# Kernel optimization log

Hardware: AMD Instinct MI355X
Metric: run time of the kernel (lower is better)

## Reference

```python
import jax, jax.numpy as jnp
import numpy as np
from jax import lax

ALPHA = 0.5
KERNEL = 25
NUM_P = 16
SEQ_LEN = 1440
PRED_LEN = 720
DWT_LEN = SEQ_LEN // 2 + 2            # 722 (pytorch_wavelets zero-mode, sym3 filt len 6)
FREQ = int(np.ceil(DWT_LEN / 2 * ALPHA) * 2)  # 362

_DEC_LO = np.array([0.035226291882100656, -0.08544127388224149, -0.13501102001039084,
                    0.4598775021193313, 0.8068915093133388, 0.3326705529509569], np.float32)
_DEC_HI = np.array([-0.3326705529509569, 0.8068915093133388, -0.4598775021193313,
                    -0.13501102001039084, 0.08544127388224149, 0.035226291882100656], np.float32)
DEC_LO, DEC_HI = jnp.asarray(_DEC_LO), jnp.asarray(_DEC_HI)
REC_LO, REC_HI = DEC_LO[::-1], DEC_HI[::-1]


def dwt1(x):
    # pytorch_wavelets DWT1DForward(J=1, mode='zero'): zero-pad then stride-2 true conv with dec filters
    B, C, L = x.shape
    out = (L + 5) // 2
    p = 2 * (out - 1) - L + 6
    xp = jnp.pad(x.reshape(B * C, 1, L), ((0, 0), (0, 0), (p // 2, p - p // 2)))
    ker = jnp.stack([DEC_LO[::-1], DEC_HI[::-1]])[:, None, :]   # (2,1,6); xcorr w/ reversed == conv
    y = lax.conv_general_dilated(xp, ker, (2,), 'VALID', dimension_numbers=('NCH', 'OIH', 'NCH'))
    return y[:, 0].reshape(B, C, out), y[:, 1].reshape(B, C, out)


def iwt1(lo, hi):
    # DWT1DInverse mode='zero': conv_transpose stride 2, padding L-2  ->  dilate + conv, pad 1
    B, C, n = lo.shape
    z = jnp.concatenate([lo.reshape(B * C, 1, n), hi.reshape(B * C, 1, n)], axis=1)
    ker = jnp.stack([REC_LO[::-1], REC_HI[::-1]])[None, :, :]   # (O=1, I=2, 6)
    y = lax.conv_general_dilated(z, ker, (1,), [(1, 1)], lhs_dilation=(2,),
                                 dimension_numbers=('NCH', 'OIH', 'NCH'))
    return y[:, 0].reshape(B, C, 2 * n - 4)


def mov_avg(x, k=KERNEL):
    pooled = lax.reduce_window(x, 0.0, lax.add, (1, 1, k), (1, 1, 1), 'VALID') / k
    return jnp.pad(pooled, ((0, 0), (0, 0), (k // 2, k // 2 - (k + 1) % 2)), mode='edge')


def mov_norm(x):
    mean = lax.stop_gradient(mov_avg(x))
    xc = lax.stop_gradient(x - mean)
    std = lax.stop_gradient(mov_avg(jnp.abs(xc))) + 1e-5
    return xc / std, mean, std


def inst_norm(x):
    mean = lax.stop_gradient(jnp.mean(x, -1, keepdims=True))
    xc = x - mean
    var = jnp.mean((xc - jnp.mean(xc, -1, keepdims=True)) ** 2, -1, keepdims=True)
    return xc / jnp.sqrt(var + 1e-5)


def mean_std_mlp(mean, std, mp, sp, mw1, mw2, sw1, sw2, mpred, spred):
    m_all = jnp.mean(mean, -1, keepdims=True)
    s_all = jnp.mean(std, -1, keepdims=True)
    mr = (mean - m_all) @ mp.T
    sr = (std - s_all) @ sp.T
    mr = jax.nn.relu(mr @ mw1.T) @ mw2.T
    sr = jax.nn.relu(sr @ sw1.T) @ sw2.T
    mean_o = mr @ mpred.T + m_all
    std_o = jax.nn.relu(sr @ spred.T + s_all) + 1e-5
    return mean_o, std_o


def forward(x, latent_w, latent_b, acp, dcp):
    xt = jnp.swapaxes(x, -1, 1)                    # (B, C, L)
    ac0, dc0 = dwt1(xt)                            # (B, C, DWT_LEN)
    ac_n = inst_norm(ac0)
    ac, m_ac, s_ac = mov_norm(ac0)
    dc, m_dc, s_dc = mov_norm(dc0)
    m_ac, s_ac = mean_std_mlp(m_ac, s_ac, *acp)    # MLPs[-1]
    m_dc, s_dc = mean_std_mlp(m_dc, s_dc, *dcp)    # MLPs[0]
    dcF = jnp.fft.fft(dc)
    acF = jnp.fft.fft(ac_n)
    idx = jnp.argsort(-jnp.abs(acF), axis=-1)[..., :FREQ]
    amp = ALPHA * jnp.take_along_axis(acF, idx, -1) + (1.0 - ALPHA) * jnp.take_along_axis(dcF, idx, -1)
    B, C, _ = dcF.shape
    bi = jnp.arange(B)[:, None, None]
    ci = jnp.arange(C)[None, :, None]
    dcF = dcF.at[bi, ci, idx].set(amp)
    dc = jnp.real(jnp.fft.ifft(dcF))
    xr = iwt1(ac, dc)                              # (B, C, SEQ_LEN)
    mean = iwt1(m_ac, m_dc)                        # (B, C, PRED_LEN)
    std = iwt1(s_ac, s_dc)
    xr = xr.reshape(B, C, NUM_P, SEQ_LEN // NUM_P)
    emb = xr @ latent_w.T + latent_b               # (B, C, NUM_P, d_model)
    return emb, mean, std


def setup_inputs() -> dict:
    key = jax.random.key(0)
    B, C = 64, 128
    d_model, d_ff = 512, 1024
    s = 0.02
    names_shapes = [
        ('x', (B, SEQ_LEN, C), 1.0),
        ('latent_w', (d_model, SEQ_LEN // NUM_P), s),
    ]
    for pre in ('ac', 'dc'):
        names_shapes += [
            (pre + '_mean_proj', (d_model, DWT_LEN), s),
            (pre + '_std_proj', (d_model, DWT_LEN), s),
            (pre + '_mean_ffn_w1', (d_ff, d_model), s),
            (pre + '_mean_ffn_w2', (d_model, d_ff), s),
            (pre + '_std_ffn_w1', (d_ff, d_model), s),
            (pre + '_std_ffn_w2', (d_model, d_ff), s),
            (pre + '_mean_pred', (PRED_LEN // 2 + 2, d_model), s),
            (pre + '_std_pred', (PRED_LEN // 2 + 2, d_model), s),
        ]
    keys = jax.random.split(key, len(names_shapes))
    inp = {n: jax.random.normal(k, shp, dtype=jnp.float32) * sc
           for (n, shp, sc), k in zip(names_shapes, keys)}
    inp['latent_b'] = jnp.zeros((d_model,), jnp.float32)
    return inp


def reference(x, latent_w, latent_b,
              ac_mean_proj, ac_std_proj, ac_mean_ffn_w1, ac_mean_ffn_w2,
              ac_std_ffn_w1, ac_std_ffn_w2, ac_mean_pred, ac_std_pred,
              dc_mean_proj, dc_std_proj, dc_mean_ffn_w1, dc_mean_ffn_w2,
              dc_std_ffn_w1, dc_std_ffn_w2, dc_mean_pred, dc_std_pred):
    acp = (ac_mean_proj, ac_std_proj, ac_mean_ffn_w1, ac_mean_ffn_w2,
           ac_std_ffn_w1, ac_std_ffn_w2, ac_mean_pred, ac_std_pred)
    dcp = (dc_mean_proj, dc_std_proj, dc_mean_ffn_w1, dc_mean_ffn_w2,
           dc_std_ffn_w1, dc_std_ffn_w2, dc_mean_pred, dc_std_pred)
    return forward(x, latent_w, latent_b, acp, dcp)
```

## Files before the change

kernel.cpp:

```cpp
#include <hip/hip_runtime.h>
#include <cmath>

#define RTOT 8192
#define NDWT 722
#define KP1  736
#define LSEQ 1440
#define NHEAD 362
#define NFREQ 362

typedef __bf16 bf16x8 __attribute__((ext_vector_type(8)));
typedef float f32x4 __attribute__((ext_vector_type(4)));
typedef float f32x2 __attribute__((ext_vector_type(2)));

__device__ __forceinline__ unsigned short f2bf(float f) {
    unsigned u = __float_as_uint(f);
    u += 0x7fffu + ((u >> 16) & 1u);
    return (unsigned short)(u >> 16);
}
__device__ __forceinline__ float bf2f(unsigned short u) {
    return __uint_as_float(((unsigned)u) << 16);
}

__device__ __forceinline__ void cmac(f32x2& s, f32x2 a, f32x2 w) {
    asm("v_pk_fma_f32 %0, %1, %2, %0 op_sel:[0,0,0] op_sel_hi:[0,1,1]\n\t"
        "v_pk_fma_f32 %0, %1, %2, %0 op_sel:[1,1,0] op_sel_hi:[1,0,1] neg_lo:[0,1,0]"
        : "+v"(s) : "v"(a), "v"(w));
}
__device__ __forceinline__ f32x2 cmul(f32x2 a, f32x2 b) {
    f32x2 r;
    asm("v_pk_mul_f32 %0, %1, %2 op_sel:[0,0] op_sel_hi:[0,1]\n\t"
        "v_pk_fma_f32 %0, %1, %2, %0 op_sel:[1,1,0] op_sel_hi:[1,0,1] neg_lo:[0,1,0]"
        : "=&v"(r) : "v"(a), "v"(b));
    return r;
}

__constant__ float c_lo[6] = {0.035226291882100656f, -0.08544127388224149f, -0.13501102001039084f,
                              0.4598775021193313f, 0.8068915093133388f, 0.3326705529509569f};
__constant__ float c_hi[6] = {-0.3326705529509569f, 0.8068915093133388f, -0.4598775021193313f,
                              -0.13501102001039084f, 0.08544127388224149f, 0.035226291882100656f};

__global__ void wtab_kernel(float2* __restrict__ Wtab) {
    int m = blockIdx.x * blockDim.x + threadIdx.x;
    if (m < NDWT) {
        double ang = -2.0 * 3.141592653589793238462643383279502884 * (double)m / (double)NDWT;
        Wtab[m] = make_float2((float)cos(ang), (float)sin(ang));
    }
}

struct CvtDesc { const float* src; unsigned short* dst; int N, K, Np, Kp; };
struct CvtArgs { CvtDesc d[17]; };
__global__ __launch_bounds__(256) void cvt_all_kernel(CvtArgs a) {
    CvtDesc d = a.d[blockIdx.y];
    int idx = blockIdx.x * 256 + threadIdx.x;
    int tot = d.Np * d.Kp;
    if (idx >= tot) return;
    int r = idx / d.Kp, c = idx - r * d.Kp;
    float v = (r < d.N && c < d.K) ? d.src[(size_t)r * d.K + c] : 0.f;
    d.dst[idx] = f2bf(v);
}

__global__ __launch_bounds__(256) void dwt_kernel(const float* __restrict__ x,
                                                  float* __restrict__ ac0,
                                                  float* __restrict__ dc0) {
    __shared__ float xs[68][129];
    const int b = blockIdx.x;
    const int t0 = blockIdx.y * 32;
    const int tid = threadIdx.x;
    const int lbase = 2 * t0 - 4;
    for (int i = tid; i < 68 * 32; i += 256) {
        int ri = i >> 5;
        int c4 = (i & 31) * 4;
        int l = lbase + ri;
        float4 v = make_float4(0.f, 0.f, 0.f, 0.f);
        if (l >= 0 && l < LSEQ)
            v = *reinterpret_cast<const float4*>(&x[((size_t)b * LSEQ + l) * 128 + c4]);
        xs[ri][c4] = v.x; xs[ri][c4 + 1] = v.y; xs[ri][c4 + 2] = v.z; xs[ri][c4 + 3] = v.w;
    }
    __syncthreads();
    const int tt = tid & 31;
    const int t = t0 + tt;
    const int cw = tid >> 5;
    if (t < NDWT) {
        #pragma unroll 4
        for (int co = 0; co < 16; co++) {
            int c = co * 8 + cw;
            float slo = 0.f, shi = 0.f;
            #pragma unroll
            for (int j = 0; j < 6; j++) {
                float v = xs[2 * tt + 5 - j][c];
                slo += v * c_lo[j];
                shi += v * c_hi[j];
            }
            size_t o = ((size_t)b * 128 + c) * NDWT + t;
            ac0[o] = slo;
            dc0[o] = shi;
        }
    }
}

__device__ __forceinline__ float blockSum256(float v, float* red) {
    #pragma unroll
    for (int o = 32; o > 0; o >>= 1) v += __shfl_down(v, o, 64);
    int lane = threadIdx.x & 63, wid = threadIdx.x >> 6;
    __syncthreads();
    if (lane == 0) red[wid] = v;
    __syncthreads();
    return red[0] + red[1] + red[2] + red[3];
}

template <bool ABS>
__device__ __forceinline__ void pool25(const float* rowv, float* pool, int tid) {
    int i0 = tid * 3;
    if (i0 < 698) {
        float s25 = 0.f;
        #pragma unroll
        for (int j = 0; j < 25; j++) { float v = rowv[i0 + j]; s25 += ABS ? fabsf(v) : v; }
        pool[i0] = s25 * (1.f / 25.f);
        #pragma unroll
        for (int qq = 1; qq < 3; qq++) {
            int i = i0 + qq;
            if (i < 698) {
                float vin = rowv[i + 24], vout = rowv[i - 1];
                s25 += (ABS ? fabsf(vin) : vin) - (ABS ? fabsf(vout) : vout);
                pool[i] = s25 * (1.f / 25.f);
            }
        }
    }
}

__global__ __launch_bounds__(256) void rowstats_kernel(
    const float* __restrict__ ac0in, const float* __restrict__ dc0in,
    float* __restrict__ acn,
    float* __restrict__ acp,
    float* __restrict__ dcp,
    unsigned short* __restrict__ cent,
    float* __restrict__ stat ) {
    __shared__ float row[NDWT];
    __shared__ float xc[NDWT];
    __shared__ float pool[698];
    __shared__ float red[4];
    const int r = blockIdx.x, tid = threadIdx.x;
    const size_t base = (size_t)r * NDWT;
    const size_t baseP = (size_t)r * KP1;
    const size_t CS = (size_t)RTOT * KP1;

    if (blockIdx.y == 0) {
        for (int i = tid; i < NDWT; i += 256) row[i] = ac0in[base + i];
        __syncthreads();
        float s = 0.f;
        for (int i = tid; i < NDWT; i += 256) s += row[i];
        float mean = blockSum256(s, red) * (1.f / 722.f);
        s = 0.f;
        for (int i = tid; i < NDWT; i += 256) s += row[i] - mean;
        float m2 = blockSum256(s, red) * (1.f / 722.f);
        s = 0.f;
        for (int i = tid; i < NDWT; i += 256) { float d = row[i] - mean - m2; s += d * d; }
        float var = blockSum256(s, red) * (1.f / 722.f);
        float inv = 1.f / sqrtf(var + 1e-5f);
        for (int i = tid; i < NDWT; i += 256) acn[base + i] = (row[i] - mean) * inv;

        pool25<false>(row, pool, tid);
        __syncthreads();
        float msum = 0.f;
        for (int l = tid; l < NDWT; l += 256) {
            int pi = l - 12; pi = pi < 0 ? 0 : (pi > 697 ? 697 : pi);
            float m = pool[pi];
            msum += m;
            xc[l] = row[l] - m;
        }
        float m_all = blockSum256(msum, red) * (1.f / 722.f);
        __syncthreads();
        pool25<true>(xc, pool, tid);
        __syncthreads();
        float ssum = 0.f;
        for (int l = tid; l < NDWT; l += 256) {
            int pi = l - 12; pi = pi < 0 ? 0 : (pi > 697 ? 697 : pi);
            float sd = pool[pi] + 1e-5f;
            ssum += sd;
            acp[base + l] = xc[l] / sd;
        }
        float s_all = blockSum256(ssum, red) * (1.f / 722.f);
        if (tid == 0) { stat[r] = m_all; stat[RTOT + r] = s_all; }
        for (int l = tid; l < KP1; l += 256) {
            if (l < NDWT) {
                float m = row[l] - xc[l];
                int pi = l - 12; pi = pi < 0 ? 0 : (pi > 697 ? 697 : pi);
                float sd = pool[pi] + 1e-5f;
                cent[baseP + l]      = f2bf(m - m_all);
                cent[CS + baseP + l] = f2bf(sd - s_all);
            } else { cent[baseP + l] = 0; cent[CS + baseP + l] = 0; }
        }
    } else {
        for (int i = tid; i < NDWT; i += 256) row[i] = dc0in[base + i];
        __syncthreads();
        pool25<false>(row, pool, tid);
        __syncthreads();
        float msum2 = 0.f;
        for (int l = tid; l < NDWT; l += 256) {
            int pi = l - 12; pi = pi < 0 ? 0 : (pi > 697 ? 697 : pi);
            float m = pool[pi];
            msum2 += m;
            xc[l] = row[l] - m;
        }
        float m_all2 = blockSum256(msum2, red) * (1.f / 722.f);
        __syncthreads();
        pool25<true>(xc, pool, tid);
        __syncthreads();
        float ssum2 = 0.f;
        for (int l = tid; l < NDWT; l += 256) {
            int pi = l - 12; pi = pi < 0 ? 0 : (pi > 697 ? 697 : pi);
            float sd = pool[pi] + 1e-5f;
            ssum2 += sd;
            dcp[base + l] = xc[l] / sd;
        }
        float s_all2 = blockSum256(ssum2, red) * (1.f / 722.f);
        if (tid == 0) { stat[2 * RTOT + r] = m_all2; stat[3 * RTOT + r] = s_all2; }
        for (int l = tid; l < KP1; l += 256) {
            if (l < NDWT) {
                float m = row[l] - xc[l];
                int pi = l - 12; pi = pi < 0 ? 0 : (pi > 697 ? 697 : pi);
                float sd = pool[pi] + 1e-5f;
                cent[2 * CS + baseP + l] = f2bf(m - m_all2);
                cent[3 * CS + baseP + l] = f2bf(sd - s_all2);
            } else { cent[2 * CS + baseP + l] = 0; cent[3 * CS + baseP + l] = 0; }
        }
    }
}

__device__ void fft722_dev(f32x2* X, f32x2* T, const f32x2* Wt, const f32x2* W19) {
    const int tid = threadIdx.x;
    if (tid < 190) {
        const int c = tid / 38;
        const int g = tid - c * 38;
        const int p = (g >= 19) ? 1 : 0;
        const int rr = g - 19 * p;
        const int t0 = c * 4;
        const int nt = (c == 4) ? 3 : 4;
        const f32x2* xp = X + 2 * rr + p;
        f32x2 st[4], w[4], s[4];
        #pragma unroll
        for (int i = 0; i < 4; i++) {
            int ti = t0 + i; if (ti > 18) ti = 0;
            st[i] = W19[ti];
            w[i] = f32x2{1.f, 0.f};
            s[i] = f32x2{0.f, 0.f};
        }
        for (int j = 0; j < 19; j++) {
            f32x2 a = xp[38 * j];
            #pragma unroll
            for (int i = 0; i < 4; i++) { cmac(s[i], a, w[i]); w[i] = cmul(w[i], st[i]); }
        }
        f32x2* Tp = T + p * 361 + rr * 19 + t0;
        #pragma unroll
        for (int i = 0; i < 4; i++) if (i < nt) Tp[i] = s[i];
    }
    __syncthreads();
    if (tid < 190) {
        const int c = tid / 38;
        const int g = tid - c * 38;
        const int p = (g >= 19) ? 1 : 0;
        const int t = g - 19 * p;
        const int j0 = c * 4;
        const int nj = (c == 4) ? 3 : 4;
        const f32x2* Tp = T + p * 361 + t;
        int kk[4];
        f32x2 st[4], w[4], s[4];
        #pragma unroll
        for (int i = 0; i < 4; i++) {
            int jj = j0 + i;
            kk[i] = (jj > 18) ? 0 : (t + 19 * jj);
            st[i] = Wt[2 * kk[i]];
            w[i] = f32x2{1.f, 0.f};
            s[i] = f32x2{0.f, 0.f};
        }
        for (int rr = 0; rr < 19; rr++) {
            f32x2 a = Tp[19 * rr];
            #pragma unroll
            for (int i = 0; i < 4; i++) { cmac(s[i], a, w[i]); w[i] = cmul(w[i], st[i]); }
        }
        f32x2* Xp = X + p * 361;
        #pragma unroll
        for (int i = 0; i < 4; i++) if (i < nj) Xp[kk[i]] = s[i];
    }
    __syncthreads();
    for (int k = tid; k < 361; k += 256) {
        f32x2 e = X[k], o = X[361 + k], w = Wt[k];
        f32x2 tt = {0.f, 0.f};
        cmac(tt, o, w);
        X[k] = e + tt;
        X[361 + k] = e - tt;
    }
    __syncthreads();
}

__global__ __launch_bounds__(256) void fft_mix_kernel(const float* __restrict__ acn,
                                                      float* __restrict__ dcp,
                                                      const f32x2* __restrict__ Wtab) {
    __shared__ f32x2 Wt[NDWT];
    __shared__ f32x2 W19s[19];
    __shared__ f32x2 B1[NDWT];
    __shared__ f32x2 B2[NDWT];
    __shared__ float smag[NDWT];
    __shared__ unsigned hist[256];
    __shared__ unsigned suf[256];
    __shared__ unsigned sh_digit, sh_rem;
    const int r = blockIdx.x, tid = threadIdx.x;
    const size_t base = (size_t)r * NDWT;

    for (int i = tid; i < NDWT; i += 256) Wt[i] = Wtab[i];
    if (tid < 19) W19s[tid] = Wtab[38 * tid];
    for (int i = tid; i < NDWT; i += 256) B1[i] = f32x2{acn[base + i], dcp[base + i]};
    __syncthreads();
    fft722_dev(B1, B2, Wt, W19s);
    for (int k = tid; k < 362; k += 256) {
        int m = (NDWT - k) % NDWT;
        f32x2 zk = B1[k], zm = B1[m];
        f32x2 ak = {0.5f * (zk.x + zm.x), 0.5f * (zk.y - zm.y)};
        f32x2 dk = {0.5f * (zk.y + zm.y), 0.5f * (zm.x - zk.x)};
        B1[k] = ak; B2[k] = dk;
        smag[k] = ak.x * ak.x + ak.y * ak.y;
        if (m != k) {
            f32x2 am = {0.5f * (zm.x + zk.x), 0.5f * (zm.y - zk.y)};
            f32x2 dm = {0.5f * (zm.y + zk.y), 0.5f * (zk.x - zm.x)};
            B1[m] = am; B2[m] = dm;
            smag[m] = am.x * am.x + am.y * am.y;
        }
    }
    __syncthreads();

    unsigned prefix = 0, rem = NFREQ;
    for (int shift = 24; shift >= 0; shift -= 8) {
        hist[tid] = 0;
        __syncthreads();
        unsigned hm = (shift == 24) ? 0u : (0xFFFFFFFFu << (shift + 8));
        for (int i = tid; i < NDWT; i += 256) {
            unsigned b = __float_as_uint(smag[i]);
            if ((b & hm) == prefix) atomicAdd(&hist[(b >> shift) & 255], 1u);
        }
        __syncthreads();
        suf[tid] = hist[tid];
        __syncthreads();
        for (int off = 1; off < 256; off <<= 1) {
            unsigned v = (tid + off < 256) ? suf[tid + off] : 0;
            __syncthreads();
            suf[tid] += v;
            __syncthreads();
        }
        unsigned Shere = suf[tid];
        unsigned Snext = (tid < 255) ? suf[tid + 1] : 0;
        if (Shere >= rem && Snext < rem) { sh_digit = (unsigned)tid; sh_rem = rem - Snext; }
        __syncthreads();
        prefix |= (sh_digit << shift);
        rem = sh_rem;
        __syncthreads();
    }
    int c0 = tid * 3, cnt = 0;
    #pragma unroll
    for (int j = 0; j < 3; j++) {
        int i = c0 + j;
        if (i < NDWT && __float_as_uint(smag[i]) == prefix) cnt++;
    }
    suf[tid] = (unsigned)cnt;
    __syncthreads();
    for (int off = 1; off < 256; off <<= 1) {
        unsigned v = (tid >= off) ? suf[tid - off] : 0;
        __syncthreads();
        suf[tid] += v;
        __syncthreads();
    }
    int myexc = (int)suf[tid] - cnt, o = 0;
    #pragma unroll
    for (int j = 0; j < 3; j++) {
        int i = c0 + j;
        if (i < NDWT) {
            unsigned b = __float_as_uint(smag[i]);
            int f = (b > prefix) ? 1 : 0;
            if (b == prefix) { if ((unsigned)(myexc + o) < rem) f = 1; o++; }
            smag[i] = f ? 1.f : 0.f;
        }
    }
    __syncthreads();

    for (int i = tid; i < NDWT; i += 256) {
        f32x2 d = B2[i];
        if (smag[i] != 0.f) { f32x2 a = B1[i]; d.x = 0.5f * (a.x + d.x); d.y = 0.5f * (a.y + d.y); }
        B1[i] = f32x2{d.x, -d.y};
    }
    __syncthreads();
    fft722_dev(B1, B2, Wt, W19s);
    for (int i = tid; i < NDWT; i += 256) dcp[base + i] = B1[i].x * (1.f / 722.f);
}

__global__ __launch_bounds__(256) void iwt_heads_kernel(const unsigned short* __restrict__ heads,
                                                        float* __restrict__ out_mean,
                                                        float* __restrict__ out_std) {
    const int z = blockIdx.z;
    const int r = blockIdx.x;
    const int t = blockIdx.y * 256 + threadIdx.x;
    if (t >= 720) return;
    const size_t HR = (size_t)RTOT * NHEAD;
    const unsigned short* lp = heads + (size_t)z * HR + (size_t)r * NHEAD;
    const unsigned short* hp = heads + (size_t)(2 + z) * HR + (size_t)r * NHEAD;
    float* out = (z ? out_std : out_mean) + (size_t)r * 720;
    float s = 0.f;
    if (t & 1) {
        int j0 = (t - 1) >> 1;
        #pragma unroll
        for (int i = 0; i < 3; i++) s += bf2f(lp[j0 + i]) * c_lo[2 * i] + bf2f(hp[j0 + i]) * c_hi[2 * i];
    } else {
        int j0 = t >> 1;
        #pragma unroll
        for (int i = 0; i < 3; i++) s += bf2f(lp[j0 + i]) * c_lo[2 * i + 1] + bf2f(hp[j0 + i]) * c_hi[2 * i + 1];
    }
    out[t] = s;
}

__global__ __launch_bounds__(256) void iwt_xr_kernel(const float* __restrict__ lo,
                                                     const float* __restrict__ hi,
                                                     unsigned short* __restrict__ xrbf) {
    const int r = blockIdx.x;
    const int t = blockIdx.y * 256 + threadIdx.x;
    if (blockIdx.y == 0 && threadIdx.x < 96) {
        int sub = threadIdx.x / 6, c = 90 + threadIdx.x % 6;
        xrbf[((size_t)r * 16 + sub) * 96 + c] = 0;
    }
    if (t >= LSEQ) return;
    const float* lp = lo + (size_t)r * NDWT;
    const float* hp = hi + (size_t)r * NDWT;
    float s = 0.f;
    if (t & 1) {
        int j0 = (t - 1) >> 1;
        #pragma unroll
        for (int i = 0; i < 3; i++) s += lp[j0 + i] * c_lo[2 * i] + hp[j0 + i] * c_hi[2 * i];
    } else {
        int j0 = t >> 1;
        #pragma unroll
        for (int i = 0; i < 3; i++) s += lp[j0 + i] * c_lo[2 * i + 1] + hp[j0 + i] * c_hi[2 * i + 1];
    }
    xrbf[((size_t)r * 16 + t / 90) * 96 + (t % 90)] = f2bf(s);
}

struct ZPtrs { const unsigned short* p[4]; };
template <int EPI>
__global__ __launch_bounds__(256) void mfma_gemm_z(
    const unsigned short* __restrict__ A, int lda, size_t zsA,
    ZPtrs Wz, int ldw,
    void* __restrict__ Cout, int ldc, size_t zsC, int Nc,
    const float* __restrict__ biasBase, const float* __restrict__ cbias,
    int Ksteps) {
    __shared__ unsigned short As[2][128 * 32];
    __shared__ unsigned short Bs[2][128 * 32];
    const int z = blockIdx.z;
    const unsigned short* Az = A + (size_t)z * zsA;
    const unsigned short* W = Wz.p[z];
    const int tid = threadIdx.x;
    const int lane = tid & 63, wid = tid >> 6;
    const int bm = blockIdx.x * 128, bn = blockIdx.y * 128;
    const int wr = (wid >> 1) * 64, wc = (wid & 1) * 64;
    f32x4 acc[4][4] = {};
    const int srow = (lane >> 2);
    const int scol = (lane & 3) * 8;
    const int ch0 = wid * 2, ch1 = wid * 2 + 1;
    const unsigned short* ga0 = Az + (size_t)(bm + ch0 * 16 + srow) * lda + scol;
    const unsigned short* ga1 = Az + (size_t)(bm + ch1 * 16 + srow) * lda + scol;
    const unsigned short* gb0 = W + (size_t)(bn + ch0 * 16 + srow) * ldw + scol;
    const unsigned short* gb1 = W + (size_t)(bn + ch1 * 16 + srow) * ldw + scol;

#define STAGE_GL(buf, ks) do { const int k0_ = (ks) * 32;                                      \
    __builtin_amdgcn_global_load_lds((const __attribute__((address_space(1))) unsigned int*)(ga0 + k0_), \
        (__attribute__((address_space(3))) unsigned int*)(&As[buf][ch0 * 512]), 16, 0, 0);     \
    __builtin_amdgcn_global_load_lds((const __attribute__((address_space(1))) unsigned int*)(gb0 + k0_), \
        (__attribute__((address_space(3))) unsigned int*)(&Bs[buf][ch0 * 512]), 16, 0, 0);     \
    __builtin_amdgcn_global_load_lds((const __attribute__((address_space(1))) unsigned int*)(ga1 + k0_), \
        (__attribute__((address_space(3))) unsigned int*)(&As[buf][ch1 * 512]), 16, 0, 0);     \
    __builtin_amdgcn_global_load_lds((const __attribute__((address_space(1))) unsigned int*)(gb1 + k0_), \
        (__attribute__((address_space(3))) unsigned int*)(&Bs[buf][ch1 * 512]), 16, 0, 0);     \
    } while (0)

    STAGE_GL(0, 0);
    int cur = 0;
    const int kof = (lane >> 4) * 8;
    for (int ks = 0; ks < Ksteps; ks++) {
        if (ks + 1 < Ksteps) {
            STAGE_GL(cur ^ 1, ks + 1);
            asm volatile("s_waitcnt vmcnt(4)" ::: "memory");
        } else {
            asm volatile("s_waitcnt vmcnt(0)" ::: "memory");
        }
        __builtin_amdgcn_s_barrier();
        __builtin_amdgcn_sched_barrier(0);
        bf16x8 af[4], bfr[4];
        #pragma unroll
        for (int m = 0; m < 4; m++)
            af[m] = *reinterpret_cast<const bf16x8*>(&As[cur][(wr + m * 16 + (lane & 15)) * 32 + kof]);
        #pragma unroll
        for (int n = 0; n < 4; n++)
            bfr[n] = *reinterpret_cast<const bf16x8*>(&Bs[cur][(wc + n * 16 + (lane & 15)) * 32 + kof]);
        #pragma unroll
        for (int m = 0; m < 4; m++)
            #pragma unroll
            for (int n = 0; n < 4; n++)
                acc[m][n] = __builtin_amdgcn_mfma_f32_16x16x32_bf16(af[m], bfr[n], acc[m][n], 0, 0, 0);
        __builtin_amdgcn_s_barrier();
        __builtin_amdgcn_sched_barrier(0);
        cur ^= 1;
    }
#undef STAGE_GL

    unsigned short* Cb = (unsigned short*)Cout + (size_t)z * zsC;
    float* Cf = (float*)Cout + (size_t)z * zsC;
    const int crow0 = bm + wr + (lane >> 4) * 4;
    const int ccol0 = bn + wc + (lane & 15);
    #pragma unroll
    for (int m = 0; m < 4; m++) {
        #pragma unroll
        for (int n = 0; n < 4; n++) {
            const int col = ccol0 + n * 16;
            if (col < Nc) {
                #pragma unroll
                for (int q = 0; q < 4; q++) {
                    const int row = crow0 + m * 16 + q;
                    float v = acc[m][n][q];
                    if (EPI == 0) {
                        Cb[(size_t)row * ldc + col] = f2bf(v);
                    } else if (EPI == 1) {
                        Cb[(size_t)row * ldc + col] = f2bf(fmaxf(v, 0.f));
                    } else if (EPI == 4) {
                        Cf[(size_t)row * ldc + col] = v + cbias[col];
                    } else {
                        float ob = biasBase[(size_t)z * RTOT + row];
                        if (z & 1) v = fmaxf(v + ob, 0.f) + 1e-5f;
                        else       v += ob;
                        Cb[(size_t)row * ldc + col] = f2bf(v);
                    }
                }
            }
        }
    }
}

extern "C" void kernel_launch(void* const* d_in, const int* in_sizes, int n_in,
                              void* d_out, int out_size, void* d_ws, size_t ws_size,
                              hipStream_t stream) {
    const float* x = (const float*)d_in[0];
    const float* latent_w = (const float*)d_in[1];
    int p0;
    const float* latent_b;
    if (n_in > 2 && in_sizes[2] == 512) { latent_b = (const float*)d_in[2]; p0 = 3; }
    else                                { latent_b = (const float*)d_in[18]; p0 = 2; }

    char* wp = (char*)d_ws;
    auto alloc = [&](size_t bytes) { char* p = wp; wp += (bytes + 255) & ~(size_t)255; return p; };
    const size_t RN = (size_t)RTOT * NDWT;
    float* acn  = (float*)alloc(RN * 4);
    float* dcb  = (float*)alloc(RN * 4);
    float* acp  = (float*)alloc(RN * 4);
    float* stat = (float*)alloc(4 * RTOT * 4);
    float2* Wtab = (float2*)alloc(NDWT * 8);
    unsigned short* cent  = (unsigned short*)alloc((size_t)4 * RTOT * KP1 * 2);
    unsigned short* mlpB4 = (unsigned short*)alloc((size_t)4 * RTOT * 512 * 2);
    unsigned short* mlpA4 = (unsigned short*)alloc((size_t)4 * RTOT * 1024 * 2);
    unsigned short* mlpC4 = (unsigned short*)alloc((size_t)4 * RTOT * 512 * 2);
    unsigned short* heads = mlpB4;
    unsigned short* xrbf = mlpC4;
    unsigned short *projW[4], *w1W[4], *w2W[4], *predW[4];
    for (int z = 0; z < 4; z++) {
        projW[z] = (unsigned short*)alloc((size_t)512 * KP1 * 2);
        w1W[z]   = (unsigned short*)alloc((size_t)1024 * 512 * 2);
        w2W[z]   = (unsigned short*)alloc((size_t)512 * 1024 * 2);
        predW[z] = (unsigned short*)alloc((size_t)384 * 512 * 2);
    }
    unsigned short* latwb = (unsigned short*)alloc((size_t)512 * 96 * 2);
    (void)ws_size;

    CvtArgs ca;
    int si = 0;
    for (int z = 0; z < 4; z++) {
        int branch = z >> 1, isStd = z & 1, wb = p0 + branch * 8;
        ca.d[si++] = {(const float*)d_in[wb + isStd],         projW[z], 512, NDWT, 512, KP1};
        ca.d[si++] = {(const float*)d_in[wb + 2 + 2 * isStd], w1W[z], 1024, 512, 1024, 512};
        ca.d[si++] = {(const float*)d_in[wb + 3 + 2 * isStd], w2W[z], 512, 1024, 512, 1024};
        ca.d[si++] = {(const float*)d_in[wb + 6 + isStd],     predW[z], NHEAD, 512, 384, 512};
    }
    ca.d[16] = {latent_w, latwb, 512, 90, 512, 96};
    cvt_all_kernel<<<dim3(2048, 17), dim3(256), 0, stream>>>(ca);

    wtab_kernel<<<dim3(3), dim3(256), 0, stream>>>(Wtab);
    dwt_kernel<<<dim3(64, 23), dim3(256), 0, stream>>>(x, acn, dcb);
    rowstats_kernel<<<dim3(RTOT, 2), dim3(256), 0, stream>>>(acn, dcb, acn, acp, dcb, cent, stat);
    fft_mix_kernel<<<dim3(RTOT), dim3(256), 0, stream>>>(acn, dcb, (const f32x2*)Wtab);

    ZPtrs Zp = {{projW[0], projW[1], projW[2], projW[3]}};
    ZPtrs Z1 = {{w1W[0], w1W[1], w1W[2], w1W[3]}};
    ZPtrs Z2 = {{w2W[0], w2W[1], w2W[2], w2W[3]}};
    ZPtrs Zh = {{predW[0], predW[1], predW[2], predW[3]}};
    mfma_gemm_z<0><<<dim3(64, 4, 4), dim3(256), 0, stream>>>(
        cent, KP1, (size_t)RTOT * KP1, Zp, KP1, mlpB4, 512, (size_t)RTOT * 512, 512, nullptr, nullptr, KP1 / 32);
    mfma_gemm_z<1><<<dim3(64, 8, 4), dim3(256), 0, stream>>>(
        mlpB4, 512, (size_t)RTOT * 512, Z1, 512, mlpA4, 1024, (size_t)RTOT * 1024, 1024, nullptr, nullptr, 16);
    mfma_gemm_z<0><<<dim3(64, 4, 4), dim3(256), 0, stream>>>(
        mlpA4, 1024, (size_t)RTOT * 1024, Z2, 1024, mlpC4, 512, (size_t)RTOT * 512, 512, nullptr, nullptr, 32);
    mfma_gemm_z<5><<<dim3(64, 3, 4), dim3(256), 0, stream>>>(
        mlpC4, 512, (size_t)RTOT * 512, Zh, 512, heads, NHEAD, (size_t)RTOT * NHEAD, NHEAD, stat, nullptr, 16);

    float* out = (float*)d_out;
    float* out_mean = out + (size_t)67108864;
    float* out_std  = out_mean + (size_t)5898240;
    iwt_heads_kernel<<<dim3(RTOT, 3, 2), dim3(256), 0, stream>>>(heads, out_mean, out_std);
    iwt_xr_kernel<<<dim3(RTOT, 6), dim3(256), 0, stream>>>(acp, dcb, xrbf);

    ZPtrs Zl = {{latwb, latwb, latwb, latwb}};
    mfma_gemm_z<4><<<dim3(1024, 4, 1), dim3(256), 0, stream>>>(
        xrbf, 96, 0, Zl, 96, out, 512, 0, 512, nullptr, latent_b, 3);
}
```

Before: 539.3 us.

## Exploit conjugate symmetry in FFT722 DFT stages and merge small kernels

Both 19-point DFT stages now pair inputs m and 19-m into sum and difference terms, so each complex MAC covers two inputs and the loop count halves. The first stage applies its twiddle on output instead of carrying it through the second stage's recurrence. The twiddle-table kernel is folded into the weight-conversion launch, and the two inverse-wavelet kernels are merged into one launch. This removes FFT arithmetic and two launches, at the cost of more complex index math and slightly different rounding.

```diff
diff --git a/kernel.cpp b/kernel.cpp
--- a/kernel.cpp
+++ b/kernel.cpp
@@ -26,6 +26,11 @@
         "v_pk_fma_f32 %0, %1, %2, %0 op_sel:[1,1,0] op_sel_hi:[1,0,1] neg_lo:[0,1,0]"
         : "+v"(s) : "v"(a), "v"(w));
 }
+__device__ __forceinline__ void cmac2(f32x2& s, f32x2 u, f32x2 v, f32x2 w) {
+    asm("v_pk_fma_f32 %0, %1, %3, %0 op_sel:[0,0,0] op_sel_hi:[1,0,1]\n\t"
+        "v_pk_fma_f32 %0, %2, %3, %0 op_sel:[1,1,0] op_sel_hi:[0,1,1] neg_lo:[0,1,0]"
+        : "+v"(s) : "v"(u), "v"(v), "v"(w));
+}
 __device__ __forceinline__ f32x2 cmul(f32x2 a, f32x2 b) {
     f32x2 r;
     asm("v_pk_mul_f32 %0, %1, %2 op_sel:[0,0] op_sel_hi:[0,1]\n\t"
@@ -39,17 +44,17 @@
 __constant__ float c_hi[6] = {-0.3326705529509569f, 0.8068915093133388f, -0.4598775021193313f,
                               -0.13501102001039084f, 0.08544127388224149f, 0.035226291882100656f};
 
-__global__ void wtab_kernel(float2* __restrict__ Wtab) {
-    int m = blockIdx.x * blockDim.x + threadIdx.x;
-    if (m < NDWT) {
-        double ang = -2.0 * 3.141592653589793238462643383279502884 * (double)m / (double)NDWT;
-        Wtab[m] = make_float2((float)cos(ang), (float)sin(ang));
-    }
-}
-
 struct CvtDesc { const float* src; unsigned short* dst; int N, K, Np, Kp; };
-struct CvtArgs { CvtDesc d[17]; };
+struct CvtArgs { CvtDesc d[17]; float2* wtab; };
 __global__ __launch_bounds__(256) void cvt_all_kernel(CvtArgs a) {
+    if (blockIdx.y == 17) {
+        int m = blockIdx.x * 256 + threadIdx.x;
+        if (m < NDWT) {
+            double ang = -2.0 * 3.141592653589793238462643383279502884 * (double)m / (double)NDWT;
+            a.wtab[m] = make_float2((float)cos(ang), (float)sin(ang));
+        }
+        return;
+    }
     CvtDesc d = a.d[blockIdx.y];
     int idx = blockIdx.x * 256 + threadIdx.x;
     int tot = d.Np * d.Kp;
@@ -134,7 +139,7 @@
     float* __restrict__ acp,
     float* __restrict__ dcp,
     unsigned short* __restrict__ cent,
-    float* __restrict__ stat ) {
+    float* __restrict__ stat) {
     __shared__ float row[NDWT];
     __shared__ float xc[NDWT];
     __shared__ float pool[698];
@@ -238,21 +243,32 @@
         const int nt = (c == 4) ? 3 : 4;
         const f32x2* xp = X + 2 * rr + p;
         f32x2 st[4], w[4], s[4];
+        f32x2 a0 = xp[0];
         #pragma unroll
         for (int i = 0; i < 4; i++) {
             int ti = t0 + i; if (ti > 18) ti = 0;
             st[i] = W19[ti];
-            w[i] = f32x2{1.f, 0.f};
-            s[i] = f32x2{0.f, 0.f};
-        }
-        for (int j = 0; j < 19; j++) {
-            f32x2 a = xp[38 * j];
-            #pragma unroll
-            for (int i = 0; i < 4; i++) { cmac(s[i], a, w[i]); w[i] = cmul(w[i], st[i]); }
-        }
+            w[i] = st[i];
+            s[i] = a0;
+        }
+        #pragma unroll
+        for (int m = 1; m <= 9; m++) {
+            f32x2 a = xp[38 * m];
+            f32x2 b = xp[38 * (19 - m)];
+            f32x2 u = a + b, v = a - b;
+            #pragma unroll
+            for (int i = 0; i < 4; i++) {
+                cmac2(s[i], u, v, w[i]);
+                if (m < 9) w[i] = cmul(w[i], st[i]);
+            }
+        }
+        int m0 = rr * t0;
         f32x2* Tp = T + p * 361 + rr * 19 + t0;
         #pragma unroll
-        for (int i = 0; i < 4; i++) if (i < nt) Tp[i] = s[i];
+        for (int i = 0; i < 4; i++) {
+            if (i < nt) Tp[i] = cmul(s[i], Wt[2 * m0]);
+            m0 += rr;
+        }
     }
     __syncthreads();
     if (tid < 190) {
@@ -260,27 +276,35 @@
         const int g = tid - c * 38;
         const int p = (g >= 19) ? 1 : 0;
         const int t = g - 19 * p;
-        const int j0 = c * 4;
+        const int jj0 = c * 4;
         const int nj = (c == 4) ? 3 : 4;
-        const f32x2* Tp = T + p * 361 + t;
-        int kk[4];
+        const f32x2* Ap = T + p * 361 + t;
         f32x2 st[4], w[4], s[4];
+        f32x2 a0 = Ap[0];
         #pragma unroll
         for (int i = 0; i < 4; i++) {
-            int jj = j0 + i;
-            kk[i] = (jj > 18) ? 0 : (t + 19 * jj);
-            st[i] = Wt[2 * kk[i]];
-            w[i] = f32x2{1.f, 0.f};
-            s[i] = f32x2{0.f, 0.f};
-        }
-        for (int rr = 0; rr < 19; rr++) {
-            f32x2 a = Tp[19 * rr];
-            #pragma unroll
-            for (int i = 0; i < 4; i++) { cmac(s[i], a, w[i]); w[i] = cmul(w[i], st[i]); }
+            int jj = jj0 + i; if (jj > 18) jj = 0;
+            st[i] = W19[jj];
+            w[i] = st[i];
+            s[i] = a0;
+        }
+        #pragma unroll
+        for (int m = 1; m <= 9; m++) {
+            f32x2 a = Ap[19 * m];
+            f32x2 b = Ap[19 * (19 - m)];
+            f32x2 u = a + b, v = a - b;
+            #pragma unroll
+            for (int i = 0; i < 4; i++) {
+                cmac2(s[i], u, v, w[i]);
+                if (m < 9) w[i] = cmul(w[i], st[i]);
+            }
         }
         f32x2* Xp = X + p * 361;
         #pragma unroll
-        for (int i = 0; i < 4; i++) if (i < nj) Xp[kk[i]] = s[i];
+        for (int i = 0; i < 4; i++) {
+            int jj = jj0 + i;
+            if (i < nj) Xp[t + 19 * jj] = s[i];
+        }
     }
     __syncthreads();
     for (int k = tid; k < 361; k += 256) {
@@ -391,53 +415,55 @@
     for (int i = tid; i < NDWT; i += 256) dcp[base + i] = B1[i].x * (1.f / 722.f);
 }
 
-__global__ __launch_bounds__(256) void iwt_heads_kernel(const unsigned short* __restrict__ heads,
-                                                        float* __restrict__ out_mean,
-                                                        float* __restrict__ out_std) {
-    const int z = blockIdx.z;
+__global__ __launch_bounds__(256) void iwt_all_kernel(const unsigned short* __restrict__ heads,
+                                                      const float* __restrict__ lo,
+                                                      const float* __restrict__ hi,
+                                                      float* __restrict__ out_mean,
+                                                      float* __restrict__ out_std,
+                                                      unsigned short* __restrict__ xrbf) {
     const int r = blockIdx.x;
-    const int t = blockIdx.y * 256 + threadIdx.x;
-    if (t >= 720) return;
-    const size_t HR = (size_t)RTOT * NHEAD;
-    const unsigned short* lp = heads + (size_t)z * HR + (size_t)r * NHEAD;
-    const unsigned short* hp = heads + (size_t)(2 + z) * HR + (size_t)r * NHEAD;
-    float* out = (z ? out_std : out_mean) + (size_t)r * 720;
-    float s = 0.f;
-    if (t & 1) {
-        int j0 = (t - 1) >> 1;
-        #pragma unroll
-        for (int i = 0; i < 3; i++) s += bf2f(lp[j0 + i]) * c_lo[2 * i] + bf2f(hp[j0 + i]) * c_hi[2 * i];
+    const int y = blockIdx.y;
+    if (y < 6) {
+        const int z = y / 3;
+        const int t = (y % 3) * 256 + threadIdx.x;
+        if (t >= 720) return;
+        const size_t HR = (size_t)RTOT * NHEAD;
+        const unsigned short* lp = heads + (size_t)z * HR + (size_t)r * NHEAD;
+        const unsigned short* hp = heads + (size_t)(2 + z) * HR + (size_t)r * NHEAD;
+        float* out = (z ? out_std : out_mean) + (size_t)r * 720;
+        float s = 0.f;
+        if (t & 1) {
+            int j0 = (t - 1) >> 1;
+            #pragma unroll
+            for (int i = 0; i < 3; i++) s += bf2f(lp[j0 + i]) * c_lo[2 * i] + bf2f(hp[j0 + i]) * c_hi[2 * i];
+        } else {
+            int j0 = t >> 1;
+            #pragma unroll
+            for (int i = 0; i < 3; i++) s += bf2f(lp[j0 + i]) * c_lo[2 * i + 1] + bf2f(hp[j0 + i]) * c_hi[2 * i + 1];
+        }
+        out[t] = s;
     } else {
-        int j0 = t >> 1;
-        #pragma unroll
-        for (int i = 0; i < 3; i++) s += bf2f(lp[j0 + i]) * c_lo[2 * i + 1] + bf2f(hp[j0 + i]) * c_hi[2 * i + 1];
-    }
-    out[t] = s;
-}
-
-__global__ __launch_bounds__(256) void iwt_xr_kernel(const float* __restrict__ lo,
-                                                     const float* __restrict__ hi,
-                                                     unsigned short* __restrict__ xrbf) {
-    const int r = blockIdx.x;
-    const int t = blockIdx.y * 256 + threadIdx.x;
-    if (blockIdx.y == 0 && threadIdx.x < 96) {
-        int sub = threadIdx.x / 6, c = 90 + threadIdx.x % 6;
-        xrbf[((size_t)r * 16 + sub) * 96 + c] = 0;
-    }
-    if (t >= LSEQ) return;
-    const float* lp = lo + (size_t)r * NDWT;
-    const float* hp = hi + (size_t)r * NDWT;
-    float s = 0.f;
-    if (t & 1) {
-        int j0 = (t - 1) >> 1;
-        #pragma unroll
-        for (int i = 0; i < 3; i++) s += lp[j0 + i] * c_lo[2 * i] + hp[j0 + i] * c_hi[2 * i];
-    } else {
-        int j0 = t >> 1;
-        #pragma unroll
-        for (int i = 0; i < 3; i++) s += lp[j0 + i] * c_lo[2 * i + 1] + hp[j0 + i] * c_hi[2 * i + 1];
-    }
-    xrbf[((size_t)r * 16 + t / 90) * 96 + (t % 90)] = f2bf(s);
+        const int yy = y - 6;
+        const int t = yy * 256 + threadIdx.x;
+        if (yy == 0 && threadIdx.x < 96) {
+            int sub = threadIdx.x / 6, c = 90 + threadIdx.x % 6;
+            xrbf[((size_t)r * 16 + sub) * 96 + c] = 0;
+        }
+        if (t >= LSEQ) return;
+        const float* lp = lo + (size_t)r * NDWT;
+        const float* hp = hi + (size_t)r * NDWT;
+        float s = 0.f;
+        if (t & 1) {
+            int j0 = (t - 1) >> 1;
+            #pragma unroll
+            for (int i = 0; i < 3; i++) s += lp[j0 + i] * c_lo[2 * i] + hp[j0 + i] * c_hi[2 * i];
+        } else {
+            int j0 = t >> 1;
+            #pragma unroll
+            for (int i = 0; i < 3; i++) s += lp[j0 + i] * c_lo[2 * i + 1] + hp[j0 + i] * c_hi[2 * i + 1];
+        }
+        xrbf[((size_t)r * 16 + t / 90) * 96 + (t % 90)] = f2bf(s);
+    }
 }
 
 struct ZPtrs { const unsigned short* p[4]; };
@@ -583,9 +609,9 @@
         ca.d[si++] = {(const float*)d_in[wb + 6 + isStd],     predW[z], NHEAD, 512, 384, 512};
     }
     ca.d[16] = {latent_w, latwb, 512, 90, 512, 96};
-    cvt_all_kernel<<<dim3(2048, 17), dim3(256), 0, stream>>>(ca);
-
-    wtab_kernel<<<dim3(3), dim3(256), 0, stream>>>(Wtab);
+    ca.wtab = Wtab;
+    cvt_all_kernel<<<dim3(2048, 18), dim3(256), 0, stream>>>(ca);
+
     dwt_kernel<<<dim3(64, 23), dim3(256), 0, stream>>>(x, acn, dcb);
     rowstats_kernel<<<dim3(RTOT, 2), dim3(256), 0, stream>>>(acn, dcb, acn, acp, dcb, cent, stat);
     fft_mix_kernel<<<dim3(RTOT), dim3(256), 0, stream>>>(acn, dcb, (const f32x2*)Wtab);
@@ -606,8 +632,7 @@
     float* out = (float*)d_out;
     float* out_mean = out + (size_t)67108864;
     float* out_std  = out_mean + (size_t)5898240;
-    iwt_heads_kernel<<<dim3(RTOT, 3, 2), dim3(256), 0, stream>>>(heads, out_mean, out_std);
-    iwt_xr_kernel<<<dim3(RTOT, 6), dim3(256), 0, stream>>>(acp, dcb, xrbf);
+    iwt_all_kernel<<<dim3(RTOT, 12), dim3(256), 0, stream>>>(heads, acp, dcb, out_mean, out_std, xrbf);
 
     ZPtrs Zl = {{latwb, latwb, latwb, latwb}};
     mfma_gemm_z<4><<<dim3(1024, 4, 1), dim3(256), 0, stream>>>(
```

After: 523.9 us. 1.03x faster.
